# Kernel optimization log

Hardware: AMD Instinct MI355X
Metric: run time of the kernel (lower is better)

## Reference

```python
import jax, jax.numpy as jnp
import numpy as np

B, N, F, H, L = 8, 4096, 240, 32, 240


def setup_inputs() -> dict:
    key = jax.random.key(0)
    k_x, k_a, k_w1, k_w2 = jax.random.split(key, 4)
    x = jax.random.normal(k_x, (B, N, F), dtype=jnp.float32)
    a = jax.random.uniform(k_a, (N, N), dtype=jnp.float32)
    W1 = jax.random.normal(k_w1, (F, H), dtype=jnp.float32) * (1.0 / np.sqrt(F))
    b1 = jnp.zeros((H,), dtype=jnp.float32)
    W2 = jax.random.normal(k_w2, (H, L), dtype=jnp.float32) * (1.0 / np.sqrt(H))
    b2 = jnp.zeros((L,), dtype=jnp.float32)
    return {"x": x, "a": a, "W1": W1, "b1": b1, "W2": W2, "b2": b2}


def reference(x, a, W1, b1, W2, b2):
    # GCNConv: transform features first (cheap), then aggregate over graph.
    h = jnp.einsum('bnf,fh->bnh', x, W1)            # [B, N, H]
    h = jnp.einsum('nm,bmh->bnh', a, h) + b1        # adjacency aggregation
    h = jax.nn.relu(h)
    # Dense linear head to label dim
    out = jnp.einsum('bnh,hl->bnl', h, W2) + b2     # [B, N, L]
    return out
```

## Files before the change

### kernel.cpp

```cpp
#include <hip/hip_runtime.h>
#include <hip/hip_bf16.h>

#define B_ 8
#define N_ 4096
#define F_ 240
#define H_ 32
#define L_ 240
#define C_ 256
#define KS 8

typedef __attribute__((ext_vector_type(8))) short bf16x8;
typedef __attribute__((ext_vector_type(4))) short bf16x4;
typedef __attribute__((ext_vector_type(4))) float f32x4;

__device__ __forceinline__ short f2bf(float f) {
    union { float f; unsigned u; } v; v.f = f;
    unsigned r = (v.u + 0x7FFFu + ((v.u >> 16) & 1u)) >> 16;
    return (short)r;
}
__device__ __forceinline__ float bf2f(short s) {
    union { unsigned u; float f; } v;
    v.u = ((unsigned)(unsigned short)s) << 16;
    return v.f;
}
__device__ __forceinline__ unsigned pk2(float a, float b) {
#if defined(__has_builtin) && __has_builtin(__builtin_amdgcn_cvt_pk_bf16_f32)
    typedef __attribute__((ext_vector_type(2))) __bf16 bfv2;
    union { bfv2 v; unsigned u; } c;
    c.v = __builtin_amdgcn_cvt_pk_bf16_f32(a, b);
    return c.u;
#else
    return (unsigned)(unsigned short)f2bf(a) | (((unsigned)(unsigned short)f2bf(b)) << 16);
#endif
}

__device__ __forceinline__ long hcf_sidx(int c, int m) {
    return ((long)(((((m >> 6) * 16 + (c >> 4)) * 2 + ((m >> 5) & 1)) * 64)
                   + ((m >> 3) & 3) * 16 + (c & 15))) * 8 + (m & 7);
}

__global__ __launch_bounds__(256) void stage1(const float* __restrict__ x,
                                              const float* __restrict__ W1,
                                              short* __restrict__ HcF) {
    __shared__ short w1t[32][264];
    __shared__ short xt[64][264];
    const int tid = threadIdx.x;
    const int b  = blockIdx.x >> 6;
    const int m0 = (blockIdx.x & 63) << 6;

    for (int idx = tid; idx < 120 * 32; idx += 256) {
        int fp = idx >> 5, h = idx & 31;
        unsigned u = pk2(W1[(2 * fp) * 32 + h], W1[(2 * fp + 1) * 32 + h]);
        *(unsigned*)&w1t[h][2 * fp] = u;
    }
    for (int idx = tid; idx < 32 * 8; idx += 256) {
        int h = idx >> 3, f = 240 + (idx & 7) * 2;
        *(unsigned*)&w1t[h][f] = 0;
    }
    const float* xb = x + ((long)b * N_ + m0) * F_;
    for (int idx = tid; idx < 64 * 60; idx += 256) {
        int row = idx / 60, c4 = idx % 60;
        float4 v = *(const float4*)(xb + row * F_ + c4 * 4);
        int2 s = make_int2((int)pk2(v.x, v.y), (int)pk2(v.z, v.w));
        *(int2*)&xt[row][c4 * 4] = s;
    }
    for (int idx = tid; idx < 64 * 2; idx += 256) {
        int row = idx >> 1, f = 240 + (idx & 1) * 8;
        int2 z = make_int2(0, 0);
        *(int2*)&xt[row][f] = z;
        *(int2*)&xt[row][f + 4] = z;
    }
    __syncthreads();

    const int w = tid >> 6, lane = tid & 63, q = lane >> 4, r = lane & 15;
    f32x4 acc0 = {0,0,0,0}, acc1 = {0,0,0,0};
#pragma unroll
    for (int kk = 0; kk < 8; ++kk) {
        bf16x8 bfr = *(const bf16x8*)&xt[w * 16 + r][kk * 32 + q * 8];
        bf16x8 a0  = *(const bf16x8*)&w1t[r][kk * 32 + q * 8];
        bf16x8 a1  = *(const bf16x8*)&w1t[16 + r][kk * 32 + q * 8];
        acc0 = __builtin_amdgcn_mfma_f32_16x16x32_bf16(a0, bfr, acc0, 0, 0, 0);
        acc1 = __builtin_amdgcn_mfma_f32_16x16x32_bf16(a1, bfr, acc1, 0, 0, 0);
    }
    const int m = m0 + w * 16 + r;
#pragma unroll
    for (int reg = 0; reg < 4; ++reg) {
        int h0 = q * 4 + reg;
        HcF[hcf_sidx(b * 32 + h0, m)]      = f2bf(acc0[reg]);
        HcF[hcf_sidx(b * 32 + 16 + h0, m)] = f2bf(acc1[reg]);
    }
}

__global__ __launch_bounds__(256, 2) void stage2(const float* __restrict__ a,
                                                 const short* __restrict__ HcF,
                                                 short* __restrict__ P) {
    __shared__ short als[2][512 * 8];
    const int tid = threadIdx.x;
    const int bm = blockIdx.x >> 3;
    const int ks = blockIdx.x & 7;
    const int m0 = bm << 6;
    const int kb0 = ks << 3;

    const int w = tid >> 6, lane = tid & 63, q = lane >> 4, r = lane & 15;
    const bf16x8* __restrict__ Hv = (const bf16x8*)HcF;

    f32x4 acc[4][4];
#pragma unroll
    for (int i = 0; i < 4; ++i)
#pragma unroll
        for (int j = 0; j < 4; ++j) acc[i][j] = (f32x4){0, 0, 0, 0};

    const int fi = tid >> 7, fkp = (tid >> 6) & 1, fq = (tid >> 4) & 3, fr = tid & 15;
    const float* aB0 = a + (long)(m0 + fi * 16 + fr) * N_ + (kb0 << 6) + fkp * 32 + fq * 8;
    const float* aB1 = aB0 + 32 * N_;
    float pre[2][16];

#define LOAD_A(bk, t)                                                          \
    {                                                                          \
        const float* s0 = aB0 + (t) * 64;                                      \
        const float* s1 = aB1 + (t) * 64;                                      \
        float4 v0 = *(const float4*)s0, v1 = *(const float4*)(s0 + 4);         \
        float4 v2 = *(const float4*)s1, v3 = *(const float4*)(s1 + 4);         \
        pre[bk][0]=v0.x;  pre[bk][1]=v0.y;  pre[bk][2]=v0.z;  pre[bk][3]=v0.w; \
        pre[bk][4]=v1.x;  pre[bk][5]=v1.y;  pre[bk][6]=v1.z;  pre[bk][7]=v1.w; \
        pre[bk][8]=v2.x;  pre[bk][9]=v2.y;  pre[bk][10]=v2.z; pre[bk][11]=v2.w;\
        pre[bk][12]=v3.x; pre[bk][13]=v3.y; pre[bk][14]=v3.z; pre[bk][15]=v3.w;\
    }
#define STORE_A(bk, buf)                                                       \
    {                                                                          \
        int4 p0 = make_int4((int)pk2(pre[bk][0],  pre[bk][1]),                 \
                            (int)pk2(pre[bk][2],  pre[bk][3]),                 \
                            (int)pk2(pre[bk][4],  pre[bk][5]),                 \
                            (int)pk2(pre[bk][6],  pre[bk][7]));                \
        int4 p1 = make_int4((int)pk2(pre[bk][8],  pre[bk][9]),                 \
                            (int)pk2(pre[bk][10], pre[bk][11]),                \
                            (int)pk2(pre[bk][12], pre[bk][13]),                \
                            (int)pk2(pre[bk][14], pre[bk][15]));               \
        *(int4*)&als[buf][tid * 8]         = p0;                               \
        *(int4*)&als[buf][(tid + 256) * 8] = p1;                               \
    }

    bf16x8 bcur[8], bnxt[8];
    LOAD_A(0, 0);
    LOAD_A(1, 1);
#pragma unroll
    for (int kp = 0; kp < 2; ++kp)
#pragma unroll
        for (int j = 0; j < 4; ++j)
            bcur[kp * 4 + j] = Hv[(long)((kb0 * 16 + w * 4 + j) * 2 + kp) * 64 + lane];
    STORE_A(0, 0);
    __syncthreads();

#pragma unroll
    for (int t = 0; t < 8; ++t) {
        const int cur = t & 1;
        if (t < 6) LOAD_A(cur, t + 2);
        if (t < 7) {
#pragma unroll
            for (int kp = 0; kp < 2; ++kp)
#pragma unroll
                for (int j = 0; j < 4; ++j)
                    bnxt[kp * 4 + j] =
                        Hv[(long)(((kb0 + t + 1) * 16 + w * 4 + j) * 2 + kp) * 64 + lane];
        }
#pragma unroll
        for (int kp = 0; kp < 2; ++kp)
#pragma unroll
            for (int i = 0; i < 4; ++i) {
                bf16x8 af = *(const bf16x8*)&als[cur][(i * 128 + kp * 64 + lane) * 8];
#pragma unroll
                for (int j = 0; j < 4; ++j)
                    acc[i][j] = __builtin_amdgcn_mfma_f32_16x16x32_bf16(
                        af, bcur[kp * 4 + j], acc[i][j], 0, 0, 0);
            }
        if (t < 7) {
            STORE_A(!cur, !cur);
#pragma unroll
            for (int u = 0; u < 8; ++u) bcur[u] = bnxt[u];
        }
        __syncthreads();
    }

#pragma unroll
    for (int i = 0; i < 4; ++i)
#pragma unroll
        for (int j = 0; j < 4; ++j) {
            int2 v = make_int2((int)pk2(acc[i][j][0], acc[i][j][1]),
                               (int)pk2(acc[i][j][2], acc[i][j][3]));
            const long F = (((long)ks * 64 + bm) * 4 + w) * 16 + i * 4 + j;
            *(int2*)&P[F * 256 + lane * 4] = v;
        }
#undef LOAD_A
#undef STORE_A
}

__global__ __launch_bounds__(256, 2) void stage2_fb(const float* __restrict__ a,
                                                    const short* __restrict__ HcF,
                                                    float* __restrict__ P) {
    __shared__ short als[512 * 8];
    const int tid = threadIdx.x;
    const int bm = blockIdx.x >> 3, ks = blockIdx.x & 7;
    const int m0 = bm << 6, kb0 = ks << 3;
    const int w = tid >> 6, lane = tid & 63, q = lane >> 4, r = lane & 15;
    const bf16x8* __restrict__ Hv = (const bf16x8*)HcF;
    f32x4 acc[4][4];
#pragma unroll
    for (int i = 0; i < 4; ++i)
#pragma unroll
        for (int j = 0; j < 4; ++j) acc[i][j] = (f32x4){0, 0, 0, 0};
    const int fi = tid >> 7, fkp = (tid >> 6) & 1, fq = (tid >> 4) & 3, fr = tid & 15;
    for (int t = 0; t < 8; ++t) {
        __syncthreads();
        for (int u = 0; u < 2; ++u) {
            const float* s = a + (long)(m0 + (fi + 2 * u) * 16 + fr) * N_
                               + ((kb0 + t) << 6) + fkp * 32 + fq * 8;
            bf16x8 sv;
            for (int e = 0; e < 8; ++e) sv[e] = f2bf(s[e]);
            *(bf16x8*)&als[(tid + u * 256) * 8] = sv;
        }
        __syncthreads();
#pragma unroll
        for (int kp = 0; kp < 2; ++kp)
#pragma unroll
            for (int i = 0; i < 4; ++i) {
                bf16x8 af = *(const bf16x8*)&als[(i * 128 + kp * 64 + lane) * 8];
#pragma unroll
                for (int j = 0; j < 4; ++j) {
                    bf16x8 bfr = Hv[(long)(((kb0 + t) * 16 + w * 4 + j) * 2 + kp) * 64 + lane];
                    acc[i][j] = __builtin_amdgcn_mfma_f32_16x16x32_bf16(af, bfr, acc[i][j], 0, 0, 0);
                }
            }
    }
#pragma unroll
    for (int i = 0; i < 4; ++i)
#pragma unroll
        for (int j = 0; j < 4; ++j) {
            const int c = w * 64 + j * 16 + r;
#pragma unroll
            for (int reg = 0; reg < 4; ++reg)
                atomicAdd(&P[(long)(m0 + i * 16 + q * 4 + reg) * C_ + c], acc[i][j][reg]);
        }
}

__global__ __launch_bounds__(512) void stage3(const short* __restrict__ P,
                                              const float* __restrict__ b1,
                                              const float* __restrict__ W2,
                                              const float* __restrict__ b2,
                                              float* __restrict__ out) {
    __shared__ short h2A[8][16][48];
    __shared__ short W2T[240][56];
    __shared__ float b2L[240];
    const int tid = threadIdx.x;
    const int bm = blockIdx.x >> 2, i = blockIdx.x & 3;
    const int n0 = (bm << 6) + (i << 4);
    const int w2 = tid >> 6, lane = tid & 63, q = lane >> 4, r = lane & 15;
    const int w = w2 >> 1, jp = w2 & 1;

    for (int idx = tid; idx < 240 * 32; idx += 512) {
        int h = idx / 240, l = idx - h * 240;
        W2T[l][h] = f2bf(W2[idx]);
    }
    if (tid < 240) b2L[tid] = b2[tid];

#pragma unroll
    for (int jj = 0; jj < 2; ++jj) {
        const int j = jp * 2 + jj;
        const int c = (w << 6) + (j << 4) + r;
        const float bb = b1[c & 31];
        float s[4] = {bb, bb, bb, bb};
        const long F0 = ((long)bm * 4 + w) * 16 + i * 4 + j;
#pragma unroll
        for (int ks = 0; ks < 8; ++ks) {
            bf16x4 v = *(const bf16x4*)&P[(F0 + (long)ks * 4096) * 256 + lane * 4];
#pragma unroll
            for (int e = 0; e < 4; ++e) s[e] += bf2f(v[e]);
        }
#pragma unroll
        for (int e = 0; e < 4; ++e) {
            float z = s[e] > 0.f ? s[e] : 0.f;
            h2A[w2][q * 4 + e][(jj << 4) + r] = f2bf(z);
        }
    }
    __syncthreads();

    bf16x8 af = *(const bf16x8*)&h2A[w2][r][q * 8];
    float* outB = out + ((long)w2 * N_ + n0) * 240;
#pragma unroll
    for (int lt = 0; lt < 15; ++lt) {
        bf16x8 bf = *(const bf16x8*)&W2T[lt * 16 + r][q * 8];
        f32x4 acc = {0, 0, 0, 0};
        acc = __builtin_amdgcn_mfma_f32_16x16x32_bf16(af, bf, acc, 0, 0, 0);
        const float bias = b2L[lt * 16 + r];
#pragma unroll
        for (int reg = 0; reg < 4; ++reg)
            outB[(long)(q * 4 + reg) * 240 + lt * 16 + r] = acc[reg] + bias;
    }
}

__global__ __launch_bounds__(256) void stage3_fb(const float* __restrict__ P,
                                                 const float* __restrict__ b1,
                                                 const float* __restrict__ W2,
                                                 const float* __restrict__ b2,
                                                 float* __restrict__ out) {
    __shared__ float h2[32][36];
    const int tid = threadIdx.x;
    const int g0 = blockIdx.x * 32;
    const int b  = g0 >> 12;
    const int n0 = g0 & 4095;
    {
        const int rr = tid >> 3, cg = tid & 7;
        const float* base = P + (long)(n0 + rr) * C_ + b * 32 + cg * 4;
        f32x4 v = *(const f32x4*)base;
        f32x4 bb = *(const f32x4*)(b1 + cg * 4);
#pragma unroll
        for (int e = 0; e < 4; ++e) {
            float s = v[e] + bb[e];
            h2[rr][cg * 4 + e] = s > 0.f ? s : 0.f;
        }
    }
    __syncthreads();
    if (tid < 240) {
        const int l = tid;
        float w2r[32];
#pragma unroll
        for (int h = 0; h < 32; ++h) w2r[h] = W2[h * 240 + l];
        const float bias = b2[l];
        for (int rr = 0; rr < 32; ++rr) {
            const f32x4* hv = (const f32x4*)h2[rr];
            float acc = bias;
#pragma unroll
            for (int hh = 0; hh < 8; ++hh) {
                f32x4 v = hv[hh];
                acc += v[0] * w2r[hh*4+0]; acc += v[1] * w2r[hh*4+1];
                acc += v[2] * w2r[hh*4+2]; acc += v[3] * w2r[hh*4+3];
            }
            out[(long)(g0 + rr) * 240 + l] = acc;
        }
    }
}

extern "C" void kernel_launch(void* const* d_in, const int* in_sizes, int n_in,
                              void* d_out, int out_size, void* d_ws, size_t ws_size,
                              hipStream_t stream) {
    const float* x  = (const float*)d_in[0];
    const float* a  = (const float*)d_in[1];
    const float* W1 = (const float*)d_in[2];
    const float* b1 = (const float*)d_in[3];
    const float* W2 = (const float*)d_in[4];
    const float* b2 = (const float*)d_in[5];
    float* out = (float*)d_out;

    short* HcF = (short*)d_ws;
    void*  P   = (void*)((char*)d_ws + (size_t)C_ * N_ * 2);
    const size_t need_main = (size_t)C_ * N_ * 2 + (size_t)KS * N_ * C_ * 2;
    const size_t need_fb   = (size_t)C_ * N_ * 2 + (size_t)N_ * C_ * 4;

    stage1<<<512, 256, 0, stream>>>(x, W1, HcF);
    if (ws_size >= need_main) {
        stage2<<<512, 256, 0, stream>>>(a, HcF, (short*)P);
        stage3<<<256, 512, 0, stream>>>((const short*)P, b1, W2, b2, out);
    } else if (ws_size >= need_fb) {
        hipMemsetAsync(P, 0, (size_t)N_ * C_ * 4, stream);
        stage2_fb<<<512, 256, 0, stream>>>(a, HcF, (float*)P);
        stage3_fb<<<1024, 256, 0, stream>>>((const float*)P, b1, W2, b2, out);
    }
}
```

Measured before the change: 164.4 us.

## Retile aggregation GEMM with 2-way split-K and smaller per-wave tiles

The adjacency aggregation kernel moves from an 8-way K split with 64-row tiles and 4x4 MFMA blocks per wave to a 2-way K split with 32-row tiles, 512-thread blocks and 2x2 MFMA blocks per wave, running 32 K steps per block. This cuts the partial-sum buffer traffic, since stage3 now reads only 2 partials instead of 8. Each thread loads a quarter of the A data per step, so register pressure drops. In exchange there are fewer blocks (256), a longer serial K loop with a barrier every step, and less data reuse per wave.

Result: slower. 175.6 us (+6.8%).

```diff
diff --git a/kernel.cpp b/kernel.cpp
--- a/kernel.cpp
+++ b/kernel.cpp
@@ -7,7 +7,7 @@
 #define H_ 32
 #define L_ 240
 #define C_ 256
-#define KS 8
+#define KS 2
 
 typedef __attribute__((ext_vector_type(8))) short bf16x8;
 typedef __attribute__((ext_vector_type(4))) short bf16x4;
@@ -91,103 +91,92 @@
     }
 }
 
-__global__ __launch_bounds__(256, 2) void stage2(const float* __restrict__ a,
+__global__ __launch_bounds__(512, 2) void stage2(const float* __restrict__ a,
                                                  const short* __restrict__ HcF,
                                                  short* __restrict__ P) {
-    __shared__ short als[2][512 * 8];
-    const int tid = threadIdx.x;
-    const int bm = blockIdx.x >> 3;
-    const int ks = blockIdx.x & 7;
-    const int m0 = bm << 6;
-    const int kb0 = ks << 3;
+    __shared__ short als[2][256 * 8];
+    const int tid = threadIdx.x;
+    const int bm = blockIdx.x >> 1;
+    const int ks = blockIdx.x & 1;
+    const int m0 = bm << 5;
+    const int kb0 = ks << 5;
 
     const int w = tid >> 6, lane = tid & 63, q = lane >> 4, r = lane & 15;
     const bf16x8* __restrict__ Hv = (const bf16x8*)HcF;
 
-    f32x4 acc[4][4];
-#pragma unroll
-    for (int i = 0; i < 4; ++i)
-#pragma unroll
-        for (int j = 0; j < 4; ++j) acc[i][j] = (f32x4){0, 0, 0, 0};
-
-    const int fi = tid >> 7, fkp = (tid >> 6) & 1, fq = (tid >> 4) & 3, fr = tid & 15;
-    const float* aB0 = a + (long)(m0 + fi * 16 + fr) * N_ + (kb0 << 6) + fkp * 32 + fq * 8;
-    const float* aB1 = aB0 + 32 * N_;
-    float pre[2][16];
+    f32x4 acc[2][2];
+#pragma unroll
+    for (int i = 0; i < 2; ++i)
+#pragma unroll
+        for (int j = 0; j < 2; ++j) acc[i][j] = (f32x4){0, 0, 0, 0};
+
+    const int f = tid >> 1, half = tid & 1;
+    const int fi = f >> 7, fkp = (f >> 6) & 1, fq = (f >> 4) & 3, fr = f & 15;
+    const float* aB = a + (long)(m0 + fi * 16 + fr) * N_
+                        + (kb0 << 6) + fkp * 32 + fq * 8 + half * 4;
+    float pre[2][4];
 
 #define LOAD_A(bk, t)                                                          \
     {                                                                          \
-        const float* s0 = aB0 + (t) * 64;                                      \
-        const float* s1 = aB1 + (t) * 64;                                      \
-        float4 v0 = *(const float4*)s0, v1 = *(const float4*)(s0 + 4);         \
-        float4 v2 = *(const float4*)s1, v3 = *(const float4*)(s1 + 4);         \
-        pre[bk][0]=v0.x;  pre[bk][1]=v0.y;  pre[bk][2]=v0.z;  pre[bk][3]=v0.w; \
-        pre[bk][4]=v1.x;  pre[bk][5]=v1.y;  pre[bk][6]=v1.z;  pre[bk][7]=v1.w; \
-        pre[bk][8]=v2.x;  pre[bk][9]=v2.y;  pre[bk][10]=v2.z; pre[bk][11]=v2.w;\
-        pre[bk][12]=v3.x; pre[bk][13]=v3.y; pre[bk][14]=v3.z; pre[bk][15]=v3.w;\
+        float4 v = *(const float4*)(aB + (t) * 64);                            \
+        pre[bk][0] = v.x; pre[bk][1] = v.y; pre[bk][2] = v.z; pre[bk][3] = v.w;\
     }
 #define STORE_A(bk, buf)                                                       \
     {                                                                          \
-        int4 p0 = make_int4((int)pk2(pre[bk][0],  pre[bk][1]),                 \
-                            (int)pk2(pre[bk][2],  pre[bk][3]),                 \
-                            (int)pk2(pre[bk][4],  pre[bk][5]),                 \
-                            (int)pk2(pre[bk][6],  pre[bk][7]));                \
-        int4 p1 = make_int4((int)pk2(pre[bk][8],  pre[bk][9]),                 \
-                            (int)pk2(pre[bk][10], pre[bk][11]),                \
-                            (int)pk2(pre[bk][12], pre[bk][13]),                \
-                            (int)pk2(pre[bk][14], pre[bk][15]));               \
-        *(int4*)&als[buf][tid * 8]         = p0;                               \
-        *(int4*)&als[buf][(tid + 256) * 8] = p1;                               \
-    }
-
-    bf16x8 bcur[8], bnxt[8];
+        int2 p = make_int2((int)pk2(pre[bk][0], pre[bk][1]),                   \
+                           (int)pk2(pre[bk][2], pre[bk][3]));                  \
+        *(int2*)&als[buf][f * 8 + half * 4] = p;                               \
+    }
+
+    bf16x8 bcur[4], bnxt[4];
     LOAD_A(0, 0);
     LOAD_A(1, 1);
 #pragma unroll
     for (int kp = 0; kp < 2; ++kp)
 #pragma unroll
-        for (int j = 0; j < 4; ++j)
-            bcur[kp * 4 + j] = Hv[(long)((kb0 * 16 + w * 4 + j) * 2 + kp) * 64 + lane];
+        for (int j = 0; j < 2; ++j)
+            bcur[kp * 2 + j] =
+                Hv[(long)((kb0 * 16 + w * 2 + j) * 2 + kp) * 64 + lane];
     STORE_A(0, 0);
     __syncthreads();
 
-#pragma unroll
-    for (int t = 0; t < 8; ++t) {
+#pragma unroll 2
+    for (int t = 0; t < 32; ++t) {
         const int cur = t & 1;
-        if (t < 6) LOAD_A(cur, t + 2);
-        if (t < 7) {
+        if (t < 30) LOAD_A(cur, t + 2);
+        if (t < 31) {
 #pragma unroll
             for (int kp = 0; kp < 2; ++kp)
 #pragma unroll
-                for (int j = 0; j < 4; ++j)
-                    bnxt[kp * 4 + j] =
-                        Hv[(long)(((kb0 + t + 1) * 16 + w * 4 + j) * 2 + kp) * 64 + lane];
+                for (int j = 0; j < 2; ++j)
+                    bnxt[kp * 2 + j] =
+                        Hv[(long)(((kb0 + t + 1) * 16 + w * 2 + j) * 2 + kp) * 64 + lane];
         }
 #pragma unroll
         for (int kp = 0; kp < 2; ++kp)
 #pragma unroll
-            for (int i = 0; i < 4; ++i) {
-                bf16x8 af = *(const bf16x8*)&als[cur][(i * 128 + kp * 64 + lane) * 8];
-#pragma unroll
-                for (int j = 0; j < 4; ++j)
+            for (int i = 0; i < 2; ++i) {
+                bf16x8 af = *(const bf16x8*)&als[cur][((i * 2 + kp) * 64 + lane) * 8];
+#pragma unroll
+                for (int j = 0; j < 2; ++j)
                     acc[i][j] = __builtin_amdgcn_mfma_f32_16x16x32_bf16(
-                        af, bcur[kp * 4 + j], acc[i][j], 0, 0, 0);
+                        af, bcur[kp * 2 + j], acc[i][j], 0, 0, 0);
             }
-        if (t < 7) {
+        if (t < 31) {
             STORE_A(!cur, !cur);
 #pragma unroll
-            for (int u = 0; u < 8; ++u) bcur[u] = bnxt[u];
+            for (int u = 0; u < 4; ++u) bcur[u] = bnxt[u];
         }
         __syncthreads();
     }
 
 #pragma unroll
-    for (int i = 0; i < 4; ++i)
-#pragma unroll
-        for (int j = 0; j < 4; ++j) {
+    for (int i = 0; i < 2; ++i)
+#pragma unroll
+        for (int j = 0; j < 2; ++j) {
             int2 v = make_int2((int)pk2(acc[i][j][0], acc[i][j][1]),
                                (int)pk2(acc[i][j][2], acc[i][j][3]));
-            const long F = (((long)ks * 64 + bm) * 4 + w) * 16 + i * 4 + j;
+            const long F = (((long)ks * 128 + bm) * 8 + w) * 4 + i * 2 + j;
             *(int2*)&P[F * 256 + lane * 4] = v;
         }
 #undef LOAD_A
@@ -251,10 +240,9 @@
     __shared__ short W2T[240][56];
     __shared__ float b2L[240];
     const int tid = threadIdx.x;
-    const int bm = blockIdx.x >> 2, i = blockIdx.x & 3;
-    const int n0 = (bm << 6) + (i << 4);
-    const int w2 = tid >> 6, lane = tid & 63, q = lane >> 4, r = lane & 15;
-    const int w = w2 >> 1, jp = w2 & 1;
+    const int g  = blockIdx.x;
+    const int n0 = g << 4;
+    const int b  = tid >> 6, lane = tid & 63, q = lane >> 4, r = lane & 15;
 
     for (int idx = tid; idx < 240 * 32; idx += 512) {
         int h = idx / 240, l = idx - h * 240;
@@ -264,27 +252,21 @@
 
 #pragma unroll
     for (int jj = 0; jj < 2; ++jj) {
-        const int j = jp * 2 + jj;
-        const int c = (w << 6) + (j << 4) + r;
-        const float bb = b1[c & 31];
-        float s[4] = {bb, bb, bb, bb};
-        const long F0 = ((long)bm * 4 + w) * 16 + i * 4 + j;
-#pragma unroll
-        for (int ks = 0; ks < 8; ++ks) {
-            bf16x4 v = *(const bf16x4*)&P[(F0 + (long)ks * 4096) * 256 + lane * 4];
-#pragma unroll
-            for (int e = 0; e < 4; ++e) s[e] += bf2f(v[e]);
-        }
+        const int h = (jj << 4) + r;
+        const float bb = b1[h];
+        const long F = ((long)(g >> 1) * 8 + b) * 4 + (g & 1) * 2 + jj;
+        bf16x4 v0 = *(const bf16x4*)&P[F * 256 + lane * 4];
+        bf16x4 v1 = *(const bf16x4*)&P[(F + 4096) * 256 + lane * 4];
 #pragma unroll
         for (int e = 0; e < 4; ++e) {
-            float z = s[e] > 0.f ? s[e] : 0.f;
-            h2A[w2][q * 4 + e][(jj << 4) + r] = f2bf(z);
+            float s = bb + bf2f(v0[e]) + bf2f(v1[e]);
+            h2A[b][q * 4 + e][h] = f2bf(s > 0.f ? s : 0.f);
         }
     }
     __syncthreads();
 
-    bf16x8 af = *(const bf16x8*)&h2A[w2][r][q * 8];
-    float* outB = out + ((long)w2 * N_ + n0) * 240;
+    bf16x8 af = *(const bf16x8*)&h2A[b][r][q * 8];
+    float* outB = out + ((long)b * N_ + n0) * 240;
 #pragma unroll
     for (int lt = 0; lt < 15; ++lt) {
         bf16x8 bf = *(const bf16x8*)&W2T[lt * 16 + r][q * 8];
@@ -357,7 +339,7 @@
 
     stage1<<<512, 256, 0, stream>>>(x, W1, HcF);
     if (ws_size >= need_main) {
-        stage2<<<512, 256, 0, stream>>>(a, HcF, (short*)P);
+        stage2<<<256, 512, 0, stream>>>(a, HcF, (short*)P);
         stage3<<<256, 512, 0, stream>>>((const short*)P, b1, W2, b2, out);
     } else if (ws_size >= need_fb) {
         hipMemsetAsync(P, 0, (size_t)N_ * C_ * 4, stream);
```
